# Kernel tuning notes

Hardware: AMD Instinct MI355X
Metric: run time of the kernel (lower is better)

The kernel has to match this reference:

```python
import jax, jax.numpy as jnp
import numpy as np

B = 64
D_IN = 4000            # reduced from hardcoded 40000 to fit memory budget (see notes)
N_NODES = 200
ADJ = N_NODES * N_NODES  # 40000 entries per adjacency
E_PER = ADJ // 4         # strictly > 0.75-quantile of 40000 continuous values == top 10000
NEG_SLOPE = 0.2          # GATv2Conv default leaky_relu slope
LN_EPS = 1e-5


def _gelu(x):
    return jax.nn.gelu(x, approximate=False)  # torch F.gelu default = exact erf


def _gatv2(x, src, dst, valid, Wl, bl, Wr, br, att, bias, heads, ch, concat, n):
    # PyG GATv2Conv (share_weights=False): xl = lin_l(x), xr = lin_r(x)
    xl = (x @ Wl + bl).reshape(n, heads, ch)
    xr = (x @ Wr + br).reshape(n, heads, ch)
    e = jax.nn.leaky_relu(xl[src] + xr[dst], NEG_SLOPE)        # [E,H,C]
    logits = jnp.einsum('ehc,hc->eh', e, att)                   # [E,H]
    if valid is not None:
        logits = jnp.where(valid[:, None], logits, -jnp.inf)
    m = jax.ops.segment_max(logits, dst, num_segments=n)
    m = jnp.where(jnp.isfinite(m), m, 0.0)
    ex = jnp.exp(logits - m[dst])
    if valid is not None:
        ex = jnp.where(valid[:, None], ex, 0.0)
    denom = jax.ops.segment_sum(ex, dst, num_segments=n)
    alpha = ex / (denom[dst] + 1e-16)                            # scatter-softmax per target
    out = jax.ops.segment_sum(xl[src] * alpha[..., None], dst, num_segments=n)
    out = out.reshape(n, heads * ch) if concat else out.mean(axis=1)
    return out + bias


def _forward(raw_fc, gbW, gbb, feW1, feb1, feW2, feb2, ln_g, ln_b,
             W1l, b1l, W1r, b1r, att1, bias1,
             W2l, b2l, W2r, b2r, att2, bias2,
             W3l, b3l, W3r, b3r, att3, bias3):
    b = raw_fc.shape[0]
    n = b * N_NODES
    # ---- build_graph ----
    adj = jax.nn.sigmoid(raw_fc @ gbW + gbb).reshape(b, N_NODES, N_NODES)
    adj = (adj + jnp.swapaxes(adj, 1, 2)) * 0.5
    means = adj.mean(axis=2)                    # [B,200]
    stds = jnp.std(adj, axis=2, ddof=1) + 1e-6  # torch std is unbiased
    base = jnp.stack([means, stds], axis=-1).reshape(n, 2)
    h = _gelu(base @ feW1 + feb1) @ feW2 + feb2
    mu = h.mean(-1, keepdims=True)
    var = h.var(-1, keepdims=True)
    x = (h - mu) / jnp.sqrt(var + LN_EPS) * ln_g + ln_b          # LayerNorm(16)
    _, idx = jax.lax.top_k(adj.reshape(b, ADJ), E_PER)           # [B, 10000]
    row = idx // N_NODES
    col = idx % N_NODES
    offs = (jnp.arange(b) * N_NODES)[:, None]
    src = (row + offs).reshape(-1)
    dst = (col + offs).reshape(-1)
    # ---- GAT stack (eval mode: dropout = identity) ----
    x = _gelu(_gatv2(x, src, dst, None, W1l, b1l, W1r, b1r, att1, bias1, 8, 128, True, n))
    # layers 2/3 have add_self_loops=True: remove existing self loops, append one per node
    loops = jnp.arange(n)
    src2 = jnp.concatenate([src, loops])
    dst2 = jnp.concatenate([dst, loops])
    valid2 = jnp.concatenate([src != dst, jnp.ones((n,), bool)])
    x = _gelu(_gatv2(x, src2, dst2, valid2, W2l, b2l, W2r, b2r, att2, bias2, 4, 256, True, n))
    x = _gelu(_gatv2(x, src2, dst2, valid2, W3l, b3l, W3r, b3r, att3, bias3, 1, 512, False, n))
    # global_mean_pool: exactly 200 nodes per graph, contiguous ordering
    return x.reshape(b, N_NODES, 512).mean(axis=1)


def setup_inputs() -> dict:
    key = jax.random.key(0)
    ks = jax.random.split(key, 16)
    f32 = jnp.float32
    def gl(k, shape, fan_in):
        return jax.random.normal(k, shape, f32) / np.sqrt(fan_in)
    inp = {}
    inp['raw_fc'] = jax.random.normal(ks[0], (B, D_IN), f32)
    inp['gbW'] = gl(ks[1], (D_IN, ADJ), D_IN)
    inp['gbb'] = jnp.zeros((ADJ,), f32)
    inp['feW1'] = gl(ks[2], (2, 8), 2);      inp['feb1'] = jnp.zeros((8,), f32)
    inp['feW2'] = gl(ks[3], (8, 16), 8);     inp['feb2'] = jnp.zeros((16,), f32)
    inp['ln_g'] = jnp.ones((16,), f32);      inp['ln_b'] = jnp.zeros((16,), f32)
    inp['W1l'] = gl(ks[4], (16, 8 * 128), 16);   inp['b1l'] = jnp.zeros((8 * 128,), f32)
    inp['W1r'] = gl(ks[5], (16, 8 * 128), 16);   inp['b1r'] = jnp.zeros((8 * 128,), f32)
    inp['att1'] = gl(ks[6], (8, 128), 128);      inp['bias1'] = jnp.zeros((8 * 128,), f32)
    inp['W2l'] = gl(ks[7], (1024, 4 * 256), 1024); inp['b2l'] = jnp.zeros((4 * 256,), f32)
    inp['W2r'] = gl(ks[8], (1024, 4 * 256), 1024); inp['b2r'] = jnp.zeros((4 * 256,), f32)
    inp['att2'] = gl(ks[9], (4, 256), 256);        inp['bias2'] = jnp.zeros((4 * 256,), f32)
    inp['W3l'] = gl(ks[10], (1024, 512), 1024);    inp['b3l'] = jnp.zeros((512,), f32)
    inp['W3r'] = gl(ks[11], (1024, 512), 1024);    inp['b3r'] = jnp.zeros((512,), f32)
    inp['att3'] = gl(ks[12], (1, 512), 512);       inp['bias3'] = jnp.zeros((512,), f32)
    return inp


def reference(raw_fc, gbW, gbb, feW1, feb1, feW2, feb2, ln_g, ln_b,
              W1l, b1l, W1r, b1r, att1, bias1,
              W2l, b2l, W2r, b2r, att2, bias2,
              W3l, b3l, W3r, b3r, att3, bias3):
    return _forward(raw_fc, gbW, gbb, feW1, feb1, feW2, feb2, ln_g, ln_b,
                    W1l, b1l, W1r, b1r, att1, bias1,
                    W2l, b2l, W2r, b2r, att2, bias2,
                    W3l, b3l, W3r, b3r, att3, bias3)
```

## Files before the change

### kernel.cpp

```cpp
#include <hip/hip_runtime.h>
#include <hip/hip_fp16.h>
#include <math.h>
#include <cstdint>
#include <cstddef>

#define NGRAPH 64
#define NN 200
#define ADJN 40000
#define DIN 4000
#define NNODE 12800

typedef float    f32x4 __attribute__((ext_vector_type(4)));
typedef _Float16 f16x8 __attribute__((ext_vector_type(8)));
typedef _Float16 f16x4 __attribute__((ext_vector_type(4)));
typedef _Float16 f16x2 __attribute__((ext_vector_type(2)));
typedef short    bf8v  __attribute__((ext_vector_type(8)));
typedef short    bf4v  __attribute__((ext_vector_type(4)));

union BF8U  { bf8v v; bf4v h[2]; };
union F16X8U{ f16x8 v; f16x4 h[2]; f16x2 p[4]; };

__device__ __forceinline__ unsigned short f2bf(float f) {
  unsigned u = __float_as_uint(f);
  return (unsigned short)((u + 0x7fffu + ((u >> 16) & 1u)) >> 16);
}
__device__ __forceinline__ float bf2f(unsigned short s) {
  return __uint_as_float(((unsigned)s) << 16);
}
__device__ __forceinline__ float gelu_f(float x) {
  return x * 0.5f * (1.0f + erff(x * 0.70710678118654752f));
}

#if defined(__has_builtin)
#if __has_builtin(__builtin_amdgcn_fdot2)
#define FDOT2(a, b, c) __builtin_amdgcn_fdot2((a), (b), (c), false)
#endif
#endif
#ifndef FDOT2
#define FDOT2(a, b, c) ((c) + (float)(a)[0] * (float)(b)[0] + (float)(a)[1] * (float)(b)[1])
#endif

__global__ __launch_bounds__(256) void prep_A(const float* __restrict__ A,
                                              short* __restrict__ Ahi,
                                              short* __restrict__ Alo) {
  const int i = blockIdx.x * 256 + threadIdx.x;
  const float v = A[i];
  const unsigned short h = f2bf(v);
  Ahi[i] = (short)h;
  Alo[i] = (short)f2bf(v - bf2f(h));
}

__global__ __launch_bounds__(256) void transp_all(
    const float* __restrict__ W2l, const float* __restrict__ W2r,
    const float* __restrict__ W3l, const float* __restrict__ W3r,
    _Float16* __restrict__ T2l, _Float16* __restrict__ T2r,
    _Float16* __restrict__ T3l, _Float16* __restrict__ T3r) {
  __shared__ float tile[32][33];
  const int z = blockIdx.z;
  if (z >= 2 && blockIdx.y >= 16) return;
  const float* src = (z == 0) ? W2l : (z == 1) ? W2r : (z == 2) ? W3l : W3r;
  _Float16* dst = (z == 0) ? T2l : (z == 1) ? T2r : (z == 2) ? T3l : T3r;
  const int N = (z < 2) ? 1024 : 512;
  const int K = 1024;
  const int bk = blockIdx.x * 32, bn = blockIdx.y * 32;
  const int tx = threadIdx.x & 31, ty = threadIdx.x >> 5;
#pragma unroll
  for (int r = 0; r < 32; r += 8) tile[ty + r][tx] = src[(size_t)(bk + ty + r) * N + bn + tx];
  __syncthreads();
#pragma unroll
  for (int r = 0; r < 32; r += 8)
    dst[(size_t)(bn + ty + r) * K + bk + tx] = (_Float16)tile[tx][ty + r];
}

#define BA_STEP(P, IT, W0, W1, AH, AL)                                          \
  {                                                                             \
    float wv[8] = {W0.x, W0.y, W0.z, W0.w, W1.x, W1.y, W1.z, W1.w};             \
    _Pragma("unroll") for (int q = 0; q < 8; ++q) {                             \
      unsigned short hh = f2bf(wv[q]);                                          \
      Wh[P][(wnc + q) * 44 + wk] = (short)hh;                                   \
      Wl[P][(wnc + q) * 44 + wk] = (short)f2bf(wv[q] - bf2f(hh));               \
    }                                                                           \
    const bf8v ahc = AH, alc = AL;                                              \
    if ((IT) + 2 < 125) {                                                       \
      const int k0 = ((IT) + 2) * 32;                                           \
      W0 = *(const float4*)(W + (size_t)(k0 + wk) * ADJN + n0 + wnc);           \
      W1 = *(const float4*)(W + (size_t)(k0 + wk) * ADJN + n0 + wnc + 4);       \
      AH = *(const bf8v*)(Ahi + (size_t)arow * DIN + k0 + kb);                  \
      AL = *(const bf8v*)(Alo + (size_t)arow * DIN + k0 + kb);                  \
    }                                                                           \
    __syncthreads();                                                            \
    _Pragma("unroll") for (int j = 0; j < 4; ++j) {                             \
      const int bc = (j * 16 + (lane & 15)) * 44 + kb;                          \
      BF8U bh, bl;                                                              \
      bh.h[0] = *(const bf4v*)(Wh[P] + bc);                                     \
      bh.h[1] = *(const bf4v*)(Wh[P] + bc + 4);                                 \
      bl.h[0] = *(const bf4v*)(Wl[P] + bc);                                     \
      bl.h[1] = *(const bf4v*)(Wl[P] + bc + 4);                                 \
      acc[j] = __builtin_amdgcn_mfma_f32_16x16x32_bf16(ahc, bh.v, acc[j], 0, 0, 0); \
      acc[j] = __builtin_amdgcn_mfma_f32_16x16x32_bf16(ahc, bl.v, acc[j], 0, 0, 0); \
      acc[j] = __builtin_amdgcn_mfma_f32_16x16x32_bf16(alc, bh.v, acc[j], 0, 0, 0); \
    }                                                                           \
  }

__global__ __launch_bounds__(256) void build_adj(
    const short* __restrict__ Ahi, const short* __restrict__ Alo,
    const float* __restrict__ W, const float* __restrict__ bias,
    float* __restrict__ adj) {
  __shared__ short Wh[2][64 * 44], Wl[2][64 * 44];
  const int t = threadIdx.x, wave = t >> 6, lane = t & 63;
  const int n0 = blockIdx.x * 64;
  const int wk = t >> 3, wnc = (t & 7) * 8;
  const int kb = (lane >> 4) * 8;
  const int arow = wave * 16 + (lane & 15);
  f32x4 acc[4] = {};
  float4 w0a = *(const float4*)(W + (size_t)wk * ADJN + n0 + wnc);
  float4 w1a = *(const float4*)(W + (size_t)wk * ADJN + n0 + wnc + 4);
  bf8v aha = *(const bf8v*)(Ahi + (size_t)arow * DIN + kb);
  bf8v ala = *(const bf8v*)(Alo + (size_t)arow * DIN + kb);
  float4 w0b = *(const float4*)(W + (size_t)(32 + wk) * ADJN + n0 + wnc);
  float4 w1b = *(const float4*)(W + (size_t)(32 + wk) * ADJN + n0 + wnc + 4);
  bf8v ahb = *(const bf8v*)(Ahi + (size_t)arow * DIN + 32 + kb);
  bf8v alb = *(const bf8v*)(Alo + (size_t)arow * DIN + 32 + kb);
  for (int it = 0; it < 124; it += 2) {
    BA_STEP(0, it, w0a, w1a, aha, ala)
    BA_STEP(1, it + 1, w0b, w1b, ahb, alb)
  }
  BA_STEP(0, 124, w0a, w1a, aha, ala)
#pragma unroll
  for (int j = 0; j < 4; ++j) {
    const int col = n0 + j * 16 + (lane & 15);
    const float bb = bias[col];
#pragma unroll
    for (int vv = 0; vv < 4; ++vv) {
      const int row = wave * 16 + (lane >> 4) * 4 + vv;
      float x = acc[j][vv] + bb;
      adj[(size_t)row * ADJN + col] = 1.0f / (1.0f + __expf(-x));
    }
  }
}

__global__ __launch_bounds__(256) void symmetrize(const float* __restrict__ adj,
                                                  float* __restrict__ adjS) {
  __shared__ float tl[64][65];
  const int g = blockIdx.x;
  const int i0 = (blockIdx.y >> 2) * 64, j0 = (blockIdx.y & 3) * 64;
  const int tx = threadIdx.x & 63, ty = threadIdx.x >> 6;
  const float* ag = adj + (size_t)g * ADJN;
#pragma unroll
  for (int r = 0; r < 64; r += 4) {
    const int jr = j0 + ty + r;
    tl[ty + r][tx] = (jr < NN && i0 + tx < NN) ? ag[jr * NN + i0 + tx] : 0.f;
  }
  __syncthreads();
#pragma unroll
  for (int r = 0; r < 64; r += 4) {
    const int i = i0 + ty + r, j = j0 + tx;
    if (i < NN && j < NN)
      adjS[(size_t)g * ADJN + i * NN + j] = 0.5f * (ag[i * NN + j] + tl[tx][ty + r]);
  }
}

__global__ __launch_bounds__(256) void rowstats(const float* __restrict__ adjS,
                                                float* __restrict__ meanv,
                                                float* __restrict__ stdv) {
  const int row = blockIdx.x * 4 + (threadIdx.x >> 6);
  const int lane = threadIdx.x & 63;
  const float* r = adjS + (size_t)row * NN;
  float s = 0.f, q = 0.f;
#pragma unroll
  for (int k = 0; k < 4; ++k) {
    int i = k * 64 + lane;
    if (i < NN) { float v = r[i]; s += v; q += v * v; }
  }
#pragma unroll
  for (int off = 32; off > 0; off >>= 1) { s += __shfl_xor(s, off); q += __shfl_xor(q, off); }
  if (lane == 0) {
    float m = s * (1.0f / 200.0f);
    float var = (q - 200.0f * m * m) * (1.0f / 199.0f);
    var = fmaxf(var, 0.f);
    meanv[row] = m;
    stdv[row] = sqrtf(var) + 1e-6f;
  }
}

__global__ __launch_bounds__(512) void radix_select(const float* __restrict__ adjS,
                                                    float* __restrict__ tau) {
  __shared__ unsigned hist[2048];
  __shared__ unsigned s_pref, s_cA;
  const int g = blockIdx.x, t = threadIdx.x, lane = t & 63;
  const float* v = adjS + (size_t)g * ADJN;
  unsigned prefix = 0, pmask = 0, cA = 0;
  const int shifts[3] = {20, 9, 0};
  const int widths[3] = {2048, 2048, 512};
  for (int pass = 0; pass < 3; ++pass) {
    const int nb = widths[pass], sh = shifts[pass];
    for (int i = t; i < nb; i += 512) hist[i] = 0u;
    __syncthreads();
    for (int e = t; e < ADJN; e += 512) {
      unsigned u = __float_as_uint(v[e]);
      if ((u & pmask) == prefix) atomicAdd(&hist[(u >> sh) & (nb - 1)], 1u);
    }
    __syncthreads();
    if (t < 64) {
      const int CH = nb >> 6;
      unsigned lsum = 0;
      for (int i = 0; i < CH; ++i) lsum += hist[t * CH + i];
      unsigned s = lsum;
#pragma unroll
      for (int off = 1; off < 64; off <<= 1) {
        unsigned o = __shfl_down(s, off);
        if (lane + off < 64) s += o;
      }
      const unsigned need = 10000u - cA;
      unsigned sn = __shfl_down(s, 1);
      const unsigned snext = (lane == 63) ? 0u : sn;
      if (s >= need && snext < need) {
        unsigned cum = snext;
        int b = t * CH;
        for (int i = CH - 1; i >= 0; --i) {
          unsigned hb = hist[t * CH + i];
          if (cum + hb >= need) { b = t * CH + i; break; }
          cum += hb;
        }
        s_pref = prefix | ((unsigned)b << sh);
        s_cA = cA + cum;
      }
    }
    __syncthreads();
    prefix = s_pref; cA = s_cA;
    pmask |= (unsigned)(widths[pass] - 1) << sh;
    __syncthreads();
  }
  if (t == 0) tau[g] = __uint_as_float(prefix);
}

__global__ __launch_bounds__(256) void node_mlp(
    const float* __restrict__ meanv, const float* __restrict__ stdv,
    const float* __restrict__ feW1, const float* __restrict__ feb1,
    const float* __restrict__ feW2, const float* __restrict__ feb2,
    const float* __restrict__ ln_g, const float* __restrict__ ln_b,
    float* __restrict__ x0) {
  const int n = blockIdx.x * 256 + threadIdx.x;
  const float mu = meanv[n], sd = stdv[n];
  float h1[8];
#pragma unroll
  for (int o = 0; o < 8; ++o) h1[o] = gelu_f(mu * feW1[o] + sd * feW1[8 + o] + feb1[o]);
  float h2[16]; float s = 0.f;
#pragma unroll
  for (int o = 0; o < 16; ++o) {
    float a = feb2[o];
#pragma unroll
    for (int k = 0; k < 8; ++k) a += h1[k] * feW2[k * 16 + o];
    h2[o] = a; s += a;
  }
  s *= (1.0f / 16.0f);
  float var = 0.f;
#pragma unroll
  for (int o = 0; o < 16; ++o) { float d = h2[o] - s; var += d * d; }
  var *= (1.0f / 16.0f);
  const float inv = 1.0f / sqrtf(var + 1e-5f);
#pragma unroll
  for (int o = 0; o < 16; ++o) x0[(size_t)n * 16 + o] = (h2[o] - s) * inv * ln_g[o] + ln_b[o];
}

__global__ __launch_bounds__(256) void build_lists(
    const float* __restrict__ adjS, const float* __restrict__ tau,
    int* __restrict__ cnt1, int* __restrict__ cnt2,
    unsigned char* __restrict__ list1, unsigned char* __restrict__ list2) {
  const int g = blockIdx.x >> 2, quad = blockIdx.x & 3;
  const float tv = tau[g];
  const int t = threadIdx.x, wave = t >> 6, lane = t & 63;
  for (int jj = wave; jj < 50; jj += 4) {
    const int j = quad * 50 + jj;
    const float* row = adjS + (size_t)g * ADJN + (size_t)j * NN;
    unsigned char* l1 = list1 + ((size_t)g * NN + j) * NN;
    unsigned char* l2 = list2 + ((size_t)g * NN + j) * NN;
    int c1 = 0, c2 = 0;
#pragma unroll
    for (int r = 0; r < 4; ++r) {
      int i = r * 64 + lane;
      bool p1 = false, p2 = false;
      if (i < NN) { float v = row[i]; p1 = (v >= tv); p2 = p1 && (i != j); }
      unsigned long long b1 = __ballot(p1);
      unsigned long long b2 = __ballot(p2);
      unsigned long long below = (lane == 0) ? 0ull : ((~0ull) >> (64 - lane));
      if (p1) l1[c1 + __popcll(b1 & below)] = (unsigned char)i;
      if (p2) l2[c2 + __popcll(b2 & below)] = (unsigned char)i;
      c1 += (int)__popcll(b1); c2 += (int)__popcll(b2);
    }
    if (lane == 0) {
      l2[c2] = (unsigned char)j;
      cnt1[g * NN + j] = c1;
      cnt2[g * NN + j] = c2 + 1;
    }
  }
}

__global__ __launch_bounds__(256) void lin16_mfma(
    const float* __restrict__ x0,
    const float* __restrict__ Wl, const float* __restrict__ bl,
    const float* __restrict__ Wr, const float* __restrict__ br,
    _Float16* __restrict__ outl, _Float16* __restrict__ outr) {
  __shared__ _Float16 Wt[2][1024 * 20];
  const int t = threadIdx.x, wave = t >> 6, lane = t & 63;
  const int mbase = blockIdx.x * 16;
  for (int i = t; i < 8192; i += 256) {
    const int mat = i >> 12, r = i & 4095;
    const int k = r >> 8, n4 = (r & 255) * 4;
    const float* Wsrc = mat ? Wr : Wl;
    float4 wv = *(const float4*)(Wsrc + (size_t)k * 1024 + n4);
    Wt[mat][(n4 + 0) * 20 + k] = (_Float16)wv.x;
    Wt[mat][(n4 + 1) * 20 + k] = (_Float16)wv.y;
    Wt[mat][(n4 + 2) * 20 + k] = (_Float16)wv.z;
    Wt[mat][(n4 + 3) * 20 + k] = (_Float16)wv.w;
  }
  const int mrow = lane & 15, kg = lane >> 4;
  F16X8U af;
#pragma unroll
  for (int q = 0; q < 8; ++q) af.v[q] = (_Float16)0.f;
  if (kg < 2) {
    const float* xp = x0 + (size_t)(mbase + mrow) * 16 + kg * 8;
    float4 v0 = *(const float4*)xp;
    float4 v1 = *(const float4*)(xp + 4);
    af.v[0] = (_Float16)v0.x; af.v[1] = (_Float16)v0.y;
    af.v[2] = (_Float16)v0.z; af.v[3] = (_Float16)v0.w;
    af.v[4] = (_Float16)v1.x; af.v[5] = (_Float16)v1.y;
    af.v[6] = (_Float16)v1.z; af.v[7] = (_Float16)v1.w;
  }
  __syncthreads();
#pragma unroll
  for (int mat = 0; mat < 2; ++mat) {
    const float* bias = mat ? br : bl;
    _Float16* out = mat ? outr : outl;
#pragma unroll
    for (int nt = 0; nt < 16; ++nt) {
      const int n0 = wave * 256 + nt * 16;
      F16X8U bfv;
#pragma unroll
      for (int q = 0; q < 8; ++q) bfv.v[q] = (_Float16)0.f;
      if (kg < 2) bfv.v = *(const f16x8*)(Wt[mat] + (n0 + mrow) * 20 + kg * 8);
      f32x4 acc = {};
      acc = __builtin_amdgcn_mfma_f32_16x16x32_f16(af.v, bfv.v, acc, 0, 0, 0);
      const int col = n0 + mrow;
      const float bb = bias[col];
#pragma unroll
      for (int j = 0; j < 4; ++j)
        out[(size_t)(mbase + kg * 4 + j) * 1024 + col] = (_Float16)(acc[j] + bb);
    }
  }
}

__global__ __launch_bounds__(256, 2) void gemm_nt(
    const _Float16* __restrict__ A,
    const _Float16* __restrict__ Bt0, const _Float16* __restrict__ Bt1,
    const float* __restrict__ b0, const float* __restrict__ b1,
    _Float16* __restrict__ out0, _Float16* __restrict__ out1,
    int Nhalf, int tilesPerHalf) {
  __shared__ _Float16 As[2][128 * 64];
  __shared__ _Float16 Bs[2][128 * 64];
  const int mbase = blockIdx.y * 128;
  const int hsel = blockIdx.x / tilesPerHalf;
  const int ncol0 = (blockIdx.x % tilesPerHalf) * 128;
  const _Float16* Bt = hsel ? Bt1 : Bt0;
  const float* bias = hsel ? b1 : b0;
  _Float16* out = hsel ? out1 : out0;
  const int t = threadIdx.x, wave = t >> 6, lane = t & 63;
  const int wm = wave >> 1, wn = wave & 1;
  f32x4 acc[4][4] = {};
  int crow[4], gco[4], sto[4];
#pragma unroll
  for (int q = 0; q < 4; ++q) {
    const int c = q * 256 + t;
    crow[q] = c >> 3;
    const int sl = c & 7;
    gco[q] = sl * 8;
    sto[q] = crow[q] * 64 + ((sl ^ (crow[q] & 7)) << 3);
  }
  f16x8 ra[4], rb[4];
#pragma unroll
  for (int q = 0; q < 4; ++q) {
    ra[q] = *(const f16x8*)(A + (size_t)(mbase + crow[q]) * 1024 + gco[q]);
    rb[q] = *(const f16x8*)(Bt + (size_t)(ncol0 + crow[q]) * 1024 + gco[q]);
  }
  for (int kt = 0; kt < 16; ++kt) {
    const int p = kt & 1;
#pragma unroll
    for (int q = 0; q < 4; ++q) {
      *(f16x8*)(As[p] + sto[q]) = ra[q];
      *(f16x8*)(Bs[p] + sto[q]) = rb[q];
    }
    if (kt < 15) {
      const int k0 = (kt + 1) * 64;
#pragma unroll
      for (int q = 0; q < 4; ++q) {
        ra[q] = *(const f16x8*)(A + (size_t)(mbase + crow[q]) * 1024 + k0 + gco[q]);
        rb[q] = *(const f16x8*)(Bt + (size_t)(ncol0 + crow[q]) * 1024 + k0 + gco[q]);
      }
    }
    __syncthreads();
#pragma unroll
    for (int ks = 0; ks < 2; ++ks) {
      F16X8U af[4], bfv[4];
#pragma unroll
      for (int m = 0; m < 4; ++m) {
        const int row = wm * 64 + m * 16 + (lane & 15);
        const int kk = ks * 32 + (lane >> 4) * 8;
        af[m].v = *(const f16x8*)(As[p] + row * 64 + (kk ^ ((row & 7) << 3)));
      }
#pragma unroll
      for (int j = 0; j < 4; ++j) {
        const int row = wn * 64 + j * 16 + (lane & 15);
        const int kk = ks * 32 + (lane >> 4) * 8;
        bfv[j].v = *(const f16x8*)(Bs[p] + row * 64 + (kk ^ ((row & 7) << 3)));
      }
#pragma unroll
      for (int j = 0; j < 4; ++j)
#pragma unroll
        for (int m = 0; m < 4; ++m)
          acc[m][j] = __builtin_amdgcn_mfma_f32_16x16x32_f16(af[m].v, bfv[j].v, acc[m][j], 0, 0, 0);
    }
  }
#pragma unroll
  for (int j = 0; j < 4; ++j) {
    const int col = ncol0 + wn * 64 + j * 16 + (lane & 15);
    const float bb = bias[col];
#pragma unroll
    for (int m = 0; m < 4; ++m) {
#pragma unroll
      for (int vv = 0; vv < 4; ++vv) {
        const int row = mbase + wm * 64 + m * 16 + (lane >> 4) * 4 + vv;
        out[(size_t)row * Nhalf + col] = (_Float16)(acc[m][j][vv] + bb);
      }
    }
  }
}

template <int C, int NR, int NSPLIT, int HC, bool USE_LL>
__global__ __launch_bounds__(1024, 4) void gat_layer(
    const _Float16* __restrict__ xlb, const _Float16* __restrict__ xrb,
    const float* __restrict__ attw, const float* __restrict__ biasw,
    const int* __restrict__ cnts, const unsigned char* __restrict__ lists,
    _Float16* __restrict__ outb) {
  extern __shared__ char smem[];
  constexpr int XLB = 200 * C * 2;
  constexpr int XRB = NR * C * 2;
  constexpr int AWB = 16 * 200 * 2;
  _Float16* xr_s = (_Float16*)(smem + XLB);
  _Float16* aw = (_Float16*)(smem + XLB + XRB);
  unsigned char* ll = (unsigned char*)(smem + XLB + XRB + AWB);
  unsigned* att_s = (unsigned*)(smem + XLB + XRB + AWB + (USE_LL ? 3200 : 0));
  const int g = blockIdx.x;
  const int hd = blockIdx.y / NSPLIT;
  const int range = blockIdx.y % NSPLIT;
  const int r0 = range * NR;
  const int t = threadIdx.x, wave = t >> 6, lane = t & 63;
  constexpr int GRP = (C == 128) ? 16 : 32;
  constexpr int NG = 64 / GRP;
  const int grp = lane / GRP, li = lane % GRP;

  for (int ch = t; ch < 200 * (C / 8); ch += 1024) {
    const int node = ch / (C / 8), cc = (ch % (C / 8)) * 8;
    f16x8 v = *(const f16x8*)(xlb + (size_t)(g * 200 + node) * HC + hd * C + cc);
    *(f16x8*)(smem + (((node * C + cc) * 2) ^ ((node & 15) << 4))) = v;
  }
  for (int ch = t; ch < NR * (C / 8); ch += 1024) {
    const int node = ch / (C / 8), cc = (ch % (C / 8)) * 8;
    *(f16x8*)(xr_s + node * C + cc) =
        *(const f16x8*)(xrb + (size_t)(g * 200 + r0 + node) * HC + hd * C + cc);
  }
  for (int i = t; i < C / 2; i += 1024) {
    f16x2 a;
    a[0] = (_Float16)attw[hd * C + 2 * i];
    a[1] = (_Float16)attw[hd * C + 2 * i + 1];
    att_s[i] = __builtin_bit_cast(unsigned, a);
  }
  __syncthreads();

  for (int jj = wave; jj < NR; jj += 16) {
    const int j = r0 + jj;
    const int gn = g * 200 + j;
    const int cnt = cnts[gn];
    const unsigned char* lst = lists + (size_t)gn * NN;
    float lg[4] = {-INFINITY, -INFINITY, -INFINITY, -INFINITY};
#pragma unroll
    for (int r = 0; r < 4; ++r) {
      const int e = (r << 6) + lane;
      if (e < cnt) {
        const int s = lst[e];
        if constexpr (USE_LL) ll[wave * 200 + e] = (unsigned char)s;
        const int swz = (s & 15) << 4;
        float accv[4] = {0.f, 0.f, 0.f, 0.f};
#pragma unroll
        for (int c0 = 0; c0 < C; c0 += 16) {
          const int ai = ((c0 >> 4) & 1) * 2;
          const unsigned* ap = att_s + c0 / 2;
          F16X8U xa, xb, raa, rbb;
          xa.v = *(const f16x8*)(smem + (((s * C + c0) * 2) ^ swz));
          xb.v = *(const f16x8*)(smem + (((s * C + c0 + 8) * 2) ^ swz));
          raa.v = *(const f16x8*)(xr_s + jj * C + c0);
          rbb.v = *(const f16x8*)(xr_s + jj * C + c0 + 8);
#pragma unroll
          for (int pq = 0; pq < 4; ++pq) {
            f16x2 z = xa.p[pq] + raa.p[pq];
            f16x2 zs = z * (_Float16)0.2f;
            f16x2 m = __builtin_elementwise_max(z, zs);
            accv[ai] = FDOT2(__builtin_bit_cast(f16x2, ap[pq]), m, accv[ai]);
            f16x2 z2 = xb.p[pq] + rbb.p[pq];
            f16x2 zs2 = z2 * (_Float16)0.2f;
            f16x2 m2 = __builtin_elementwise_max(z2, zs2);
            accv[ai + 1] = FDOT2(__builtin_bit_cast(f16x2, ap[4 + pq]), m2, accv[ai + 1]);
          }
        }
        lg[r] = (accv[0] + accv[1]) + (accv[2] + accv[3]);
      }
    }
    float mloc = fmaxf(fmaxf(lg[0], lg[1]), fmaxf(lg[2], lg[3]));
#pragma unroll
    for (int off = 32; off > 0; off >>= 1) mloc = fmaxf(mloc, __shfl_xor(mloc, off));
    float ex[4]; float ps = 0.f;
#pragma unroll
    for (int r = 0; r < 4; ++r) { ex[r] = __expf(lg[r] - mloc); ps += ex[r]; }
#pragma unroll
    for (int off = 32; off > 0; off >>= 1) ps += __shfl_xor(ps, off);
    const float denom = ps + 1e-16f;
#pragma unroll
    for (int r = 0; r < 4; ++r) {
      const int e = (r << 6) + lane;
      if (e < cnt) aw[wave * 200 + e] = (_Float16)(ex[r] / denom);
    }
    float o[8] = {};
    for (int e0 = 0; e0 < cnt; e0 += NG) {
      const int e = e0 + grp;
      if (e < cnt) {
        const float a = (float)aw[wave * 200 + e];
        int s;
        if constexpr (USE_LL) s = ll[wave * 200 + e]; else s = lst[e];
        const int swz = (s & 15) << 4;
        f16x8 xv = *(const f16x8*)(smem + (((s * C + li * 8) * 2) ^ swz));
#pragma unroll
        for (int q = 0; q < 8; ++q) o[q] += a * (float)xv[q];
      }
    }
#pragma unroll
    for (int q = 0; q < 8; ++q) {
      if constexpr (GRP == 16) o[q] += __shfl_xor(o[q], 16);
      o[q] += __shfl_xor(o[q], 32);
    }
    if (grp == 0) {
      const int colb = hd * C + li * 8;
      f16x8 ov;
#pragma unroll
      for (int q = 0; q < 8; ++q) ov[q] = (_Float16)gelu_f(o[q] + biasw[colb + q]);
      *(f16x8*)(outb + (size_t)gn * HC + colb) = ov;
    }
  }
}

__global__ __launch_bounds__(1024, 4) void gat_l3(
    const _Float16* __restrict__ xlb, const _Float16* __restrict__ xrb,
    const float* __restrict__ attw, const float* __restrict__ biasw,
    const int* __restrict__ cnts, const unsigned char* __restrict__ lists,
    float* __restrict__ psum) {
  extern __shared__ char smem[];
  _Float16* xr_s = (_Float16*)(smem + 51200);
  float* plog = (float*)(smem + 64000);
  unsigned* att_s = (unsigned*)(smem + 104000);
  const int g = blockIdx.x, range = blockIdx.y, r0 = range * 50;
  const int t = threadIdx.x, wave = t >> 6, lane = t & 63;
  const int grp = lane >> 4, li = lane & 15;

  for (int chunk = 0; chunk < 4; ++chunk) {
    if (chunk) __syncthreads();
    for (int ch = t; ch < 200 * 16; ch += 1024) {
      const int node = ch >> 4, cc = (ch & 15) * 8;
      *(f16x8*)(smem + (((node * 128 + cc) * 2) ^ ((node & 15) << 4))) =
          *(const f16x8*)(xlb + (size_t)(g * 200 + node) * 512 + chunk * 128 + cc);
    }
    for (int ch = t; ch < 50 * 16; ch += 1024) {
      const int node = ch >> 4, cc = (ch & 15) * 8;
      *(f16x8*)(xr_s + node * 128 + cc) =
          *(const f16x8*)(xrb + (size_t)(g * 200 + r0 + node) * 512 + chunk * 128 + cc);
    }
    for (int i = t; i < 64; i += 1024) {
      f16x2 a;
      a[0] = (_Float16)attw[chunk * 128 + 2 * i];
      a[1] = (_Float16)attw[chunk * 128 + 2 * i + 1];
      att_s[i] = __builtin_bit_cast(unsigned, a);
    }
    __syncthreads();
    for (int jj = wave; jj < 50; jj += 16) {
      const int gn = g * 200 + r0 + jj;
      const int cnt = cnts[gn];
      const unsigned char* lst = lists + (size_t)gn * NN;
#pragma unroll
      for (int r = 0; r < 4; ++r) {
        const int e = (r << 6) + lane;
        if (e < cnt) {
          const int s = lst[e];
          const int swz = (s & 15) << 4;
          float accv[4] = {0.f, 0.f, 0.f, 0.f};
#pragma unroll
          for (int c0 = 0; c0 < 128; c0 += 16) {
            const int ai = ((c0 >> 4) & 1) * 2;
            const unsigned* ap = att_s + c0 / 2;
            F16X8U xa, xb, raa, rbb;
            xa.v = *(const f16x8*)(smem + (((s * 128 + c0) * 2) ^ swz));
            xb.v = *(const f16x8*)(smem + (((s * 128 + c0 + 8) * 2) ^ swz));
            raa.v = *(const f16x8*)(xr_s + jj * 128 + c0);
            rbb.v = *(const f16x8*)(xr_s + jj * 128 + c0 + 8);
#pragma unroll
            for (int pq = 0; pq < 4; ++pq) {
              f16x2 z = xa.p[pq] + raa.p[pq];
              f16x2 zs = z * (_Float16)0.2f;
              f16x2 m = __builtin_elementwise_max(z, zs);
              accv[ai] = FDOT2(__builtin_bit_cast(f16x2, ap[pq]), m, accv[ai]);
              f16x2 z2 = xb.p[pq] + rbb.p[pq];
              f16x2 zs2 = z2 * (_Float16)0.2f;
              f16x2 m2 = __builtin_elementwise_max(z2, zs2);
              accv[ai + 1] = FDOT2(__builtin_bit_cast(f16x2, ap[4 + pq]), m2, accv[ai + 1]);
            }
          }
          const float acc = (accv[0] + accv[1]) + (accv[2] + accv[3]);
          if (chunk == 0) plog[jj * 200 + e] = acc;
          else plog[jj * 200 + e] += acc;
        }
      }
    }
  }
  __syncthreads();
  for (int jj = wave; jj < 50; jj += 16) {
    const int gn = g * 200 + r0 + jj;
    const int cnt = cnts[gn];
    float lg[4] = {-INFINITY, -INFINITY, -INFINITY, -INFINITY};
#pragma unroll
    for (int r = 0; r < 4; ++r) {
      const int e = (r << 6) + lane;
      if (e < cnt) lg[r] = plog[jj * 200 + e];
    }
    float mloc = fmaxf(fmaxf(lg[0], lg[1]), fmaxf(lg[2], lg[3]));
#pragma unroll
    for (int off = 32; off > 0; off >>= 1) mloc = fmaxf(mloc, __shfl_xor(mloc, off));
    float ex[4]; float ps = 0.f;
#pragma unroll
    for (int r = 0; r < 4; ++r) { ex[r] = __expf(lg[r] - mloc); ps += ex[r]; }
#pragma unroll
    for (int off = 32; off > 0; off >>= 1) ps += __shfl_xor(ps, off);
    const float denom = ps + 1e-16f;
#pragma unroll
    for (int r = 0; r < 4; ++r) {
      const int e = (r << 6) + lane;
      if (e < cnt) plog[jj * 200 + e] = ex[r] / denom;
    }
  }
  for (int chunk = 0; chunk < 4; ++chunk) {
    __syncthreads();
    for (int ch = t; ch < 200 * 16; ch += 1024) {
      const int node = ch >> 4, cc = (ch & 15) * 8;
      *(f16x8*)(smem + (((node * 128 + cc) * 2) ^ ((node & 15) << 4))) =
          *(const f16x8*)(xlb + (size_t)(g * 200 + node) * 512 + chunk * 128 + cc);
    }
    __syncthreads();
    float p[8] = {};
    for (int jj = wave; jj < 50; jj += 16) {
      const int gn = g * 200 + r0 + jj;
      const int cnt = cnts[gn];
      const unsigned char* lst = lists + (size_t)gn * NN;
      float o[8] = {};
      for (int e0 = 0; e0 < cnt; e0 += 4) {
        const int e = e0 + grp;
        if (e < cnt) {
          const float a = plog[jj * 200 + e];
          const int s = lst[e];
          const int swz = (s & 15) << 4;
          f16x8 xv = *(const f16x8*)(smem + (((s * 128 + li * 8) * 2) ^ swz));
#pragma unroll
          for (int q = 0; q < 8; ++q) o[q] += a * (float)xv[q];
        }
      }
#pragma unroll
      for (int q = 0; q < 8; ++q) {
        o[q] += __shfl_xor(o[q], 16);
        o[q] += __shfl_xor(o[q], 32);
      }
      if (grp == 0) {
        const int colb = chunk * 128 + li * 8;
#pragma unroll
        for (int q = 0; q < 8; ++q) p[q] += gelu_f(o[q] + biasw[colb + q]);
      }
    }
    if (grp == 0) {
      const int slot = range * 16 + wave;
      float* pd = psum + ((size_t)slot * 64 + g) * 512 + chunk * 128 + li * 8;
      float4 a0 = {p[0], p[1], p[2], p[3]};
      float4 a1 = {p[4], p[5], p[6], p[7]};
      *(float4*)pd = a0;
      *(float4*)(pd + 4) = a1;
    }
  }
}

__global__ void finalize(const float* __restrict__ psum, float* __restrict__ out) {
  const int idx = blockIdx.x * 256 + threadIdx.x;
  float s = 0.f;
#pragma unroll
  for (int k = 0; k < 64; ++k) s += psum[(size_t)k * 32768 + idx];
  out[idx] = s * 0.005f;
}

extern "C" void kernel_launch(void* const* d_in, const int* in_sizes, int n_in,
                              void* d_out, int out_size, void* d_ws, size_t ws_size,
                              hipStream_t stream) {
  const float* raw_fc = (const float*)d_in[0];
  const float* gbW = (const float*)d_in[1];
  const float* gbb = (const float*)d_in[2];
  const float* feW1 = (const float*)d_in[3];
  const float* feb1 = (const float*)d_in[4];
  const float* feW2 = (const float*)d_in[5];
  const float* feb2 = (const float*)d_in[6];
  const float* ln_g = (const float*)d_in[7];
  const float* ln_b = (const float*)d_in[8];
  const float* W1l = (const float*)d_in[9];  const float* b1l = (const float*)d_in[10];
  const float* W1r = (const float*)d_in[11]; const float* b1r = (const float*)d_in[12];
  const float* att1 = (const float*)d_in[13]; const float* bias1 = (const float*)d_in[14];
  const float* W2l = (const float*)d_in[15]; const float* b2l = (const float*)d_in[16];
  const float* W2r = (const float*)d_in[17]; const float* b2r = (const float*)d_in[18];
  const float* att2 = (const float*)d_in[19]; const float* bias2 = (const float*)d_in[20];
  const float* W3l = (const float*)d_in[21]; const float* b3l = (const float*)d_in[22];
  const float* W3r = (const float*)d_in[23]; const float* b3r = (const float*)d_in[24];
  const float* att3 = (const float*)d_in[25]; const float* bias3 = (const float*)d_in[26];

  if (ws_size < 121000000) return;

  char* w = (char*)d_ws;
  float* adj   = (float*)(w + 0);
  float* adjS  = (float*)(w + 10240000);
  float* meanv = (float*)(w + 20480000);
  float* stdv  = (float*)(w + 20531200);
  float* tau   = (float*)(w + 20582400);
  float* x0    = (float*)(w + 20582656);
  int* cnt1    = (int*)(w + 21401856);
  int* cnt2    = (int*)(w + 21453056);
  unsigned char* list1 = (unsigned char*)(w + 21504256);
  unsigned char* list2 = (unsigned char*)(w + 24064256);
  _Float16* bufA = (_Float16*)(w + 26624256);
  _Float16* bufB = (_Float16*)(w + 52838656);
  _Float16* bufC = (_Float16*)(w + 79053056);
  float* psum = (float*)(w + 105267456);
  short* Ahi  = (short*)(w + 113656064);
  short* Alo  = (short*)(w + 114168064);
  _Float16* Wt2l = (_Float16*)(w + 114680064);
  _Float16* Wt2r = (_Float16*)(w + 116777216);
  _Float16* Wt3l = (_Float16*)(w + 118874368);
  _Float16* Wt3r = (_Float16*)(w + 119922944);

  const int SMEM_L1 = 112256;
  const int SMEM_L2 = 160512;
  const int SMEM_L3 = 104256;
  hipFuncSetAttribute((const void*)gat_layer<128, 200, 1, 1024, true>,
                      hipFuncAttributeMaxDynamicSharedMemorySize, SMEM_L1);
  hipFuncSetAttribute((const void*)gat_layer<256, 100, 2, 1024, false>,
                      hipFuncAttributeMaxDynamicSharedMemorySize, SMEM_L2);
  hipFuncSetAttribute((const void*)gat_l3,
                      hipFuncAttributeMaxDynamicSharedMemorySize, SMEM_L3);

  prep_A<<<1000, 256, 0, stream>>>(raw_fc, Ahi, Alo);
  transp_all<<<dim3(32, 32, 4), 256, 0, stream>>>(W2l, W2r, W3l, W3r, Wt2l, Wt2r, Wt3l, Wt3r);
  build_adj<<<625, 256, 0, stream>>>(Ahi, Alo, gbW, gbb, adj);
  symmetrize<<<dim3(64, 16), 256, 0, stream>>>(adj, adjS);
  rowstats<<<3200, 256, 0, stream>>>(adjS, meanv, stdv);
  radix_select<<<64, 512, 0, stream>>>(adjS, tau);
  node_mlp<<<50, 256, 0, stream>>>(meanv, stdv, feW1, feb1, feW2, feb2, ln_g, ln_b, x0);
  build_lists<<<256, 256, 0, stream>>>(adjS, tau, cnt1, cnt2, list1, list2);
  lin16_mfma<<<800, 256, 0, stream>>>(x0, W1l, b1l, W1r, b1r, bufA, bufB);
  gat_layer<128, 200, 1, 1024, true><<<dim3(64, 8), 1024, SMEM_L1, stream>>>(
      bufA, bufB, att1, bias1, cnt1, list1, bufC);
  gemm_nt<<<dim3(16, 100), 256, 0, stream>>>(bufC, Wt2l, Wt2r, b2l, b2r, bufA, bufB, 1024, 8);
  gat_layer<256, 100, 2, 1024, false><<<dim3(64, 8), 1024, SMEM_L2, stream>>>(
      bufA, bufB, att2, bias2, cnt2, list2, bufC);
  gemm_nt<<<dim3(8, 100), 256, 0, stream>>>(bufC, Wt3l, Wt3r, b3l, b3r, bufA, bufB, 512, 4);
  gat_l3<<<dim3(64, 4), 1024, SMEM_L3, stream>>>(bufA, bufB, att3, bias3, cnt2, list2, psum);
  finalize<<<128, 256, 0, stream>>>(psum, (float*)d_out);
}
```

Baseline: 1.009 ms.

## Fuse radix select with list building, fuse node MLP into lin16, restructure pipelines

Merges radix_select and build_lists into one kernel that builds edge lists right after finding the threshold, and uses four privatized histogram copies with 1024 threads. Folds node_mlp into the layer-1 linear kernel, and halves that kernel's shared weight buffer by loading Wl and Wr in turn. Reorders build_adj so the bf16 split conversion of the next tile overlaps the current MFMAs, and moves gemm_nt's prefetch to after the barrier. gat_layer now streams xr rows through a per-wave register buffer instead of staging them in shared memory, dropping the NSPLIT split, so layer 2 runs one block per head with less shared memory. These remove launches and intermediate buffers, but the fused list kernel has only 64 blocks.

```diff
diff --git a/kernel.cpp b/kernel.cpp
--- a/kernel.cpp
+++ b/kernel.cpp
@@ -72,35 +72,34 @@
     dst[(size_t)(bn + ty + r) * K + bk + tx] = (_Float16)tile[tx][ty + r];
 }
 
-#define BA_STEP(P, IT, W0, W1, AH, AL)                                          \
-  {                                                                             \
-    float wv[8] = {W0.x, W0.y, W0.z, W0.w, W1.x, W1.y, W1.z, W1.w};             \
+#define BA_CONV(PB, W0, W1)                                                     \
+  { float wv[8] = {W0.x, W0.y, W0.z, W0.w, W1.x, W1.y, W1.z, W1.w};             \
     _Pragma("unroll") for (int q = 0; q < 8; ++q) {                             \
       unsigned short hh = f2bf(wv[q]);                                          \
-      Wh[P][(wnc + q) * 44 + wk] = (short)hh;                                   \
-      Wl[P][(wnc + q) * 44 + wk] = (short)f2bf(wv[q] - bf2f(hh));               \
-    }                                                                           \
-    const bf8v ahc = AH, alc = AL;                                              \
-    if ((IT) + 2 < 125) {                                                       \
-      const int k0 = ((IT) + 2) * 32;                                           \
-      W0 = *(const float4*)(W + (size_t)(k0 + wk) * ADJN + n0 + wnc);           \
-      W1 = *(const float4*)(W + (size_t)(k0 + wk) * ADJN + n0 + wnc + 4);       \
-      AH = *(const bf8v*)(Ahi + (size_t)arow * DIN + k0 + kb);                  \
-      AL = *(const bf8v*)(Alo + (size_t)arow * DIN + k0 + kb);                  \
-    }                                                                           \
-    __syncthreads();                                                            \
-    _Pragma("unroll") for (int j = 0; j < 4; ++j) {                             \
-      const int bc = (j * 16 + (lane & 15)) * 44 + kb;                          \
-      BF8U bh, bl;                                                              \
-      bh.h[0] = *(const bf4v*)(Wh[P] + bc);                                     \
-      bh.h[1] = *(const bf4v*)(Wh[P] + bc + 4);                                 \
-      bl.h[0] = *(const bf4v*)(Wl[P] + bc);                                     \
-      bl.h[1] = *(const bf4v*)(Wl[P] + bc + 4);                                 \
-      acc[j] = __builtin_amdgcn_mfma_f32_16x16x32_bf16(ahc, bh.v, acc[j], 0, 0, 0); \
-      acc[j] = __builtin_amdgcn_mfma_f32_16x16x32_bf16(ahc, bl.v, acc[j], 0, 0, 0); \
-      acc[j] = __builtin_amdgcn_mfma_f32_16x16x32_bf16(alc, bh.v, acc[j], 0, 0, 0); \
-    }                                                                           \
-  }
+      Wh[PB][(wnc + q) * 44 + wk] = (short)hh;                                  \
+      Wl[PB][(wnc + q) * 44 + wk] = (short)f2bf(wv[q] - bf2f(hh));              \
+    } }
+
+#define BA_MFMA(PB, AHC, ALC)                                                   \
+  _Pragma("unroll") for (int j = 0; j < 4; ++j) {                               \
+    const int bc = (j * 16 + (lane & 15)) * 44 + kb;                            \
+    BF8U bh, bl;                                                                \
+    bh.h[0] = *(const bf4v*)(Wh[PB] + bc);                                      \
+    bh.h[1] = *(const bf4v*)(Wh[PB] + bc + 4);                                  \
+    bl.h[0] = *(const bf4v*)(Wl[PB] + bc);                                      \
+    bl.h[1] = *(const bf4v*)(Wl[PB] + bc + 4);                                  \
+    acc[j] = __builtin_amdgcn_mfma_f32_16x16x32_bf16(AHC, bh.v, acc[j], 0, 0, 0); \
+    acc[j] = __builtin_amdgcn_mfma_f32_16x16x32_bf16(AHC, bl.v, acc[j], 0, 0, 0); \
+    acc[j] = __builtin_amdgcn_mfma_f32_16x16x32_bf16(ALC, bh.v, acc[j], 0, 0, 0); \
+  }
+
+#define BA_LOADW(W0, W1, K0)                                                    \
+  W0 = *(const float4*)(W + (size_t)((K0) + wk) * ADJN + n0 + wnc);             \
+  W1 = *(const float4*)(W + (size_t)((K0) + wk) * ADJN + n0 + wnc + 4);
+
+#define BA_LOADA(AH, AL, K0)                                                    \
+  AH = *(const bf8v*)(Ahi + (size_t)arow * DIN + (K0) + kb);                    \
+  AL = *(const bf8v*)(Alo + (size_t)arow * DIN + (K0) + kb);
 
 __global__ __launch_bounds__(256) void build_adj(
     const short* __restrict__ Ahi, const short* __restrict__ Alo,
@@ -113,19 +112,39 @@
   const int kb = (lane >> 4) * 8;
   const int arow = wave * 16 + (lane & 15);
   f32x4 acc[4] = {};
-  float4 w0a = *(const float4*)(W + (size_t)wk * ADJN + n0 + wnc);
-  float4 w1a = *(const float4*)(W + (size_t)wk * ADJN + n0 + wnc + 4);
-  bf8v aha = *(const bf8v*)(Ahi + (size_t)arow * DIN + kb);
-  bf8v ala = *(const bf8v*)(Alo + (size_t)arow * DIN + kb);
-  float4 w0b = *(const float4*)(W + (size_t)(32 + wk) * ADJN + n0 + wnc);
-  float4 w1b = *(const float4*)(W + (size_t)(32 + wk) * ADJN + n0 + wnc + 4);
-  bf8v ahb = *(const bf8v*)(Ahi + (size_t)arow * DIN + 32 + kb);
-  bf8v alb = *(const bf8v*)(Alo + (size_t)arow * DIN + 32 + kb);
+  float4 w0s0, w1s0, w0s1, w1s1;
+  bf8v ahs0, als0, ahs1, als1;
+  BA_LOADW(w0s0, w1s0, 0)
+  BA_LOADA(ahs0, als0, 0)
+  BA_LOADW(w0s1, w1s1, 32)
+  BA_LOADA(ahs1, als1, 32)
+  BA_CONV(0, w0s0, w1s0)
   for (int it = 0; it < 124; it += 2) {
-    BA_STEP(0, it, w0a, w1a, aha, ala)
-    BA_STEP(1, it + 1, w0b, w1b, ahb, alb)
-  }
-  BA_STEP(0, 124, w0a, w1a, aha, ala)
+    __syncthreads();
+    {
+      const bf8v ahc = ahs0, alc = als0;
+      if (it + 2 < 125) {
+        const int k2 = (it + 2) * 32;
+        BA_LOADW(w0s0, w1s0, k2)
+        BA_LOADA(ahs0, als0, k2)
+      }
+      BA_MFMA(0, ahc, alc)
+      BA_CONV(1, w0s1, w1s1)
+    }
+    __syncthreads();
+    {
+      const bf8v ahc = ahs1, alc = als1;
+      if (it + 3 < 125) {
+        const int k2 = (it + 3) * 32;
+        BA_LOADW(w0s1, w1s1, k2)
+        BA_LOADA(ahs1, als1, k2)
+      }
+      BA_MFMA(1, ahc, alc)
+      if (it + 2 < 125) BA_CONV(0, w0s0, w1s0)
+    }
+  }
+  __syncthreads();
+  BA_MFMA(0, ahs0, als0)
 #pragma unroll
   for (int j = 0; j < 4; ++j) {
     const int col = n0 + j * 16 + (lane & 15);
@@ -183,28 +202,34 @@
   }
 }
 
-__global__ __launch_bounds__(512) void radix_select(const float* __restrict__ adjS,
-                                                    float* __restrict__ tau) {
-  __shared__ unsigned hist[2048];
+__global__ __launch_bounds__(1024) void radix_lists(
+    const float* __restrict__ adjS,
+    int* __restrict__ cnt1, int* __restrict__ cnt2,
+    unsigned char* __restrict__ list1, unsigned char* __restrict__ list2) {
+  __shared__ unsigned hist[4 * 2048];
   __shared__ unsigned s_pref, s_cA;
-  const int g = blockIdx.x, t = threadIdx.x, lane = t & 63;
+  const int g = blockIdx.x, t = threadIdx.x, lane = t & 63, wave = t >> 6;
   const float* v = adjS + (size_t)g * ADJN;
   unsigned prefix = 0, pmask = 0, cA = 0;
   const int shifts[3] = {20, 9, 0};
   const int widths[3] = {2048, 2048, 512};
   for (int pass = 0; pass < 3; ++pass) {
     const int nb = widths[pass], sh = shifts[pass];
-    for (int i = t; i < nb; i += 512) hist[i] = 0u;
-    __syncthreads();
-    for (int e = t; e < ADJN; e += 512) {
+    for (int i = t; i < 8192; i += 1024) hist[i] = 0u;
+    __syncthreads();
+    const int cpy = (lane & 3) * 2048;
+    for (int e = t; e < ADJN; e += 1024) {
       unsigned u = __float_as_uint(v[e]);
-      if ((u & pmask) == prefix) atomicAdd(&hist[(u >> sh) & (nb - 1)], 1u);
+      if ((u & pmask) == prefix) atomicAdd(&hist[cpy + ((u >> sh) & (nb - 1))], 1u);
     }
     __syncthreads();
     if (t < 64) {
       const int CH = nb >> 6;
       unsigned lsum = 0;
-      for (int i = 0; i < CH; ++i) lsum += hist[t * CH + i];
+      for (int i = 0; i < CH; ++i) {
+        const int b = t * CH + i;
+        lsum += hist[b] + hist[2048 + b] + hist[4096 + b] + hist[6144 + b];
+      }
       unsigned s = lsum;
 #pragma unroll
       for (int off = 1; off < 64; off <<= 1) {
@@ -216,13 +241,14 @@
       const unsigned snext = (lane == 63) ? 0u : sn;
       if (s >= need && snext < need) {
         unsigned cum = snext;
-        int b = t * CH;
+        int bsel = t * CH;
         for (int i = CH - 1; i >= 0; --i) {
-          unsigned hb = hist[t * CH + i];
-          if (cum + hb >= need) { b = t * CH + i; break; }
+          const int b = t * CH + i;
+          unsigned hb = hist[b] + hist[2048 + b] + hist[4096 + b] + hist[6144 + b];
+          if (cum + hb >= need) { bsel = b; break; }
           cum += hb;
         }
-        s_pref = prefix | ((unsigned)b << sh);
+        s_pref = prefix | ((unsigned)bsel << sh);
         s_cA = cA + cum;
       }
     }
@@ -231,47 +257,8 @@
     pmask |= (unsigned)(widths[pass] - 1) << sh;
     __syncthreads();
   }
-  if (t == 0) tau[g] = __uint_as_float(prefix);
-}
-
-__global__ __launch_bounds__(256) void node_mlp(
-    const float* __restrict__ meanv, const float* __restrict__ stdv,
-    const float* __restrict__ feW1, const float* __restrict__ feb1,
-    const float* __restrict__ feW2, const float* __restrict__ feb2,
-    const float* __restrict__ ln_g, const float* __restrict__ ln_b,
-    float* __restrict__ x0) {
-  const int n = blockIdx.x * 256 + threadIdx.x;
-  const float mu = meanv[n], sd = stdv[n];
-  float h1[8];
-#pragma unroll
-  for (int o = 0; o < 8; ++o) h1[o] = gelu_f(mu * feW1[o] + sd * feW1[8 + o] + feb1[o]);
-  float h2[16]; float s = 0.f;
-#pragma unroll
-  for (int o = 0; o < 16; ++o) {
-    float a = feb2[o];
-#pragma unroll
-    for (int k = 0; k < 8; ++k) a += h1[k] * feW2[k * 16 + o];
-    h2[o] = a; s += a;
-  }
-  s *= (1.0f / 16.0f);
-  float var = 0.f;
-#pragma unroll
-  for (int o = 0; o < 16; ++o) { float d = h2[o] - s; var += d * d; }
-  var *= (1.0f / 16.0f);
-  const float inv = 1.0f / sqrtf(var + 1e-5f);
-#pragma unroll
-  for (int o = 0; o < 16; ++o) x0[(size_t)n * 16 + o] = (h2[o] - s) * inv * ln_g[o] + ln_b[o];
-}
-
-__global__ __launch_bounds__(256) void build_lists(
-    const float* __restrict__ adjS, const float* __restrict__ tau,
-    int* __restrict__ cnt1, int* __restrict__ cnt2,
-    unsigned char* __restrict__ list1, unsigned char* __restrict__ list2) {
-  const int g = blockIdx.x >> 2, quad = blockIdx.x & 3;
-  const float tv = tau[g];
-  const int t = threadIdx.x, wave = t >> 6, lane = t & 63;
-  for (int jj = wave; jj < 50; jj += 4) {
-    const int j = quad * 50 + jj;
+  const float tv = __uint_as_float(prefix);
+  for (int j = wave; j < NN; j += 16) {
     const float* row = adjS + (size_t)g * ADJN + (size_t)j * NN;
     unsigned char* l1 = list1 + ((size_t)g * NN + j) * NN;
     unsigned char* l2 = list2 + ((size_t)g * NN + j) * NN;
@@ -280,7 +267,7 @@
     for (int r = 0; r < 4; ++r) {
       int i = r * 64 + lane;
       bool p1 = false, p2 = false;
-      if (i < NN) { float v = row[i]; p1 = (v >= tv); p2 = p1 && (i != j); }
+      if (i < NN) { float vv = row[i]; p1 = (vv >= tv); p2 = p1 && (i != j); }
       unsigned long long b1 = __ballot(p1);
       unsigned long long b2 = __ballot(p2);
       unsigned long long below = (lane == 0) ? 0ull : ((~0ull) >> (64 - lane));
@@ -296,40 +283,60 @@
   }
 }
 
-__global__ __launch_bounds__(256) void lin16_mfma(
-    const float* __restrict__ x0,
+__global__ __launch_bounds__(256) void lin16_fused(
+    const float* __restrict__ meanv, const float* __restrict__ stdv,
+    const float* __restrict__ feW1, const float* __restrict__ feb1,
+    const float* __restrict__ feW2, const float* __restrict__ feb2,
+    const float* __restrict__ ln_g, const float* __restrict__ ln_b,
     const float* __restrict__ Wl, const float* __restrict__ bl,
     const float* __restrict__ Wr, const float* __restrict__ br,
     _Float16* __restrict__ outl, _Float16* __restrict__ outr) {
-  __shared__ _Float16 Wt[2][1024 * 20];
+  __shared__ _Float16 Wt[1024 * 20];
+  __shared__ float x0s[16][17];
   const int t = threadIdx.x, wave = t >> 6, lane = t & 63;
   const int mbase = blockIdx.x * 16;
-  for (int i = t; i < 8192; i += 256) {
-    const int mat = i >> 12, r = i & 4095;
-    const int k = r >> 8, n4 = (r & 255) * 4;
-    const float* Wsrc = mat ? Wr : Wl;
-    float4 wv = *(const float4*)(Wsrc + (size_t)k * 1024 + n4);
-    Wt[mat][(n4 + 0) * 20 + k] = (_Float16)wv.x;
-    Wt[mat][(n4 + 1) * 20 + k] = (_Float16)wv.y;
-    Wt[mat][(n4 + 2) * 20 + k] = (_Float16)wv.z;
-    Wt[mat][(n4 + 3) * 20 + k] = (_Float16)wv.w;
-  }
+  {
+    const int n = t >> 4, o = t & 15;
+    const float mu = meanv[mbase + n], sd = stdv[mbase + n];
+    float h1[8];
+#pragma unroll
+    for (int k = 0; k < 8; ++k) h1[k] = gelu_f(mu * feW1[k] + sd * feW1[8 + k] + feb1[k]);
+    float h2 = feb2[o];
+#pragma unroll
+    for (int k = 0; k < 8; ++k) h2 += h1[k] * feW2[k * 16 + o];
+    float s = h2;
+#pragma unroll
+    for (int off = 1; off < 16; off <<= 1) s += __shfl_xor(s, off);
+    s *= (1.0f / 16.0f);
+    const float d = h2 - s;
+    float vv = d * d;
+#pragma unroll
+    for (int off = 1; off < 16; off <<= 1) vv += __shfl_xor(vv, off);
+    vv *= (1.0f / 16.0f);
+    x0s[n][o] = d * (1.0f / sqrtf(vv + 1e-5f)) * ln_g[o] + ln_b[o];
+  }
+  __syncthreads();
   const int mrow = lane & 15, kg = lane >> 4;
   F16X8U af;
 #pragma unroll
   for (int q = 0; q < 8; ++q) af.v[q] = (_Float16)0.f;
   if (kg < 2) {
-    const float* xp = x0 + (size_t)(mbase + mrow) * 16 + kg * 8;
-    float4 v0 = *(const float4*)xp;
-    float4 v1 = *(const float4*)(xp + 4);
-    af.v[0] = (_Float16)v0.x; af.v[1] = (_Float16)v0.y;
-    af.v[2] = (_Float16)v0.z; af.v[3] = (_Float16)v0.w;
-    af.v[4] = (_Float16)v1.x; af.v[5] = (_Float16)v1.y;
-    af.v[6] = (_Float16)v1.z; af.v[7] = (_Float16)v1.w;
-  }
-  __syncthreads();
+#pragma unroll
+    for (int q = 0; q < 8; ++q) af.v[q] = (_Float16)x0s[mrow][kg * 8 + q];
+  }
 #pragma unroll
   for (int mat = 0; mat < 2; ++mat) {
+    if (mat) __syncthreads();
+    const float* Wsrc = mat ? Wr : Wl;
+    for (int i = t; i < 4096; i += 256) {
+      const int k = i >> 8, n4 = (i & 255) * 4;
+      float4 wv = *(const float4*)(Wsrc + (size_t)k * 1024 + n4);
+      Wt[(n4 + 0) * 20 + k] = (_Float16)wv.x;
+      Wt[(n4 + 1) * 20 + k] = (_Float16)wv.y;
+      Wt[(n4 + 2) * 20 + k] = (_Float16)wv.z;
+      Wt[(n4 + 3) * 20 + k] = (_Float16)wv.w;
+    }
+    __syncthreads();
     const float* bias = mat ? br : bl;
     _Float16* out = mat ? outr : outl;
 #pragma unroll
@@ -338,7 +345,7 @@
       F16X8U bfv;
 #pragma unroll
       for (int q = 0; q < 8; ++q) bfv.v[q] = (_Float16)0.f;
-      if (kg < 2) bfv.v = *(const f16x8*)(Wt[mat] + (n0 + mrow) * 20 + kg * 8);
+      if (kg < 2) bfv.v = *(const f16x8*)(Wt + (n0 + mrow) * 20 + kg * 8);
       f32x4 acc = {};
       acc = __builtin_amdgcn_mfma_f32_16x16x32_f16(af.v, bfv.v, acc, 0, 0, 0);
       const int col = n0 + mrow;
@@ -389,6 +396,7 @@
       *(f16x8*)(As[p] + sto[q]) = ra[q];
       *(f16x8*)(Bs[p] + sto[q]) = rb[q];
     }
+    __syncthreads();
     if (kt < 15) {
       const int k0 = (kt + 1) * 64;
 #pragma unroll
@@ -397,7 +405,6 @@
         rb[q] = *(const f16x8*)(Bt + (size_t)(ncol0 + crow[q]) * 1024 + k0 + gco[q]);
       }
     }
-    __syncthreads();
 #pragma unroll
     for (int ks = 0; ks < 2; ++ks) {
       F16X8U af[4], bfv[4];
@@ -435,7 +442,7 @@
   }
 }
 
-template <int C, int NR, int NSPLIT, int HC, bool USE_LL>
+template <int C, int HC, bool USE_LL>
 __global__ __launch_bounds__(1024, 4) void gat_layer(
     const _Float16* __restrict__ xlb, const _Float16* __restrict__ xrb,
     const float* __restrict__ attw, const float* __restrict__ biasw,
@@ -443,16 +450,13 @@
     _Float16* __restrict__ outb) {
   extern __shared__ char smem[];
   constexpr int XLB = 200 * C * 2;
-  constexpr int XRB = NR * C * 2;
-  constexpr int AWB = 16 * 200 * 2;
+  constexpr int XRW = 16 * C * 2;
   _Float16* xr_s = (_Float16*)(smem + XLB);
-  _Float16* aw = (_Float16*)(smem + XLB + XRB);
-  unsigned char* ll = (unsigned char*)(smem + XLB + XRB + AWB);
-  unsigned* att_s = (unsigned*)(smem + XLB + XRB + AWB + (USE_LL ? 3200 : 0));
+  _Float16* aw = (_Float16*)(smem + XLB + XRW);
+  unsigned char* ll = (unsigned char*)(smem + XLB + XRW + 6400);
+  unsigned* att_s = (unsigned*)(smem + XLB + XRW + 6400 + (USE_LL ? 3200 : 0));
   const int g = blockIdx.x;
-  const int hd = blockIdx.y / NSPLIT;
-  const int range = blockIdx.y % NSPLIT;
-  const int r0 = range * NR;
+  const int hd = blockIdx.y;
   const int t = threadIdx.x, wave = t >> 6, lane = t & 63;
   constexpr int GRP = (C == 128) ? 16 : 32;
   constexpr int NG = 64 / GRP;
@@ -462,11 +466,6 @@
     const int node = ch / (C / 8), cc = (ch % (C / 8)) * 8;
     f16x8 v = *(const f16x8*)(xlb + (size_t)(g * 200 + node) * HC + hd * C + cc);
     *(f16x8*)(smem + (((node * C + cc) * 2) ^ ((node & 15) << 4))) = v;
-  }
-  for (int ch = t; ch < NR * (C / 8); ch += 1024) {
-    const int node = ch / (C / 8), cc = (ch % (C / 8)) * 8;
-    *(f16x8*)(xr_s + node * C + cc) =
-        *(const f16x8*)(xrb + (size_t)(g * 200 + r0 + node) * HC + hd * C + cc);
   }
   for (int i = t; i < C / 2; i += 1024) {
     f16x2 a;
@@ -476,11 +475,20 @@
   }
   __syncthreads();
 
-  for (int jj = wave; jj < NR; jj += 16) {
-    const int j = r0 + jj;
-    const int gn = g * 200 + j;
+  _Float16* xr_w = xr_s + wave * C;
+  f16x8 xrreg;
+  if (lane < C / 8)
+    xrreg = *(const f16x8*)(xrb + (size_t)(g * 200 + wave) * HC + hd * C + lane * 8);
+
+  for (int jj = wave; jj < 200; jj += 16) {
+    const int gn = g * 200 + jj;
     const int cnt = cnts[gn];
     const unsigned char* lst = lists + (size_t)gn * NN;
+    if (lane < C / 8) {
+      *(f16x8*)(xr_w + lane * 8) = xrreg;
+      if (jj + 16 < 200)
+        xrreg = *(const f16x8*)(xrb + (size_t)(gn + 16) * HC + hd * C + lane * 8);
+    }
     float lg[4] = {-INFINITY, -INFINITY, -INFINITY, -INFINITY};
 #pragma unroll
     for (int r = 0; r < 4; ++r) {
@@ -497,8 +505,8 @@
           F16X8U xa, xb, raa, rbb;
           xa.v = *(const f16x8*)(smem + (((s * C + c0) * 2) ^ swz));
           xb.v = *(const f16x8*)(smem + (((s * C + c0 + 8) * 2) ^ swz));
-          raa.v = *(const f16x8*)(xr_s + jj * C + c0);
-          rbb.v = *(const f16x8*)(xr_s + jj * C + c0 + 8);
+          raa.v = *(const f16x8*)(xr_w + c0);
+          rbb.v = *(const f16x8*)(xr_w + c0 + 8);
 #pragma unroll
           for (int pq = 0; pq < 4; ++pq) {
             f16x2 z = xa.p[pq] + raa.p[pq];
@@ -736,8 +744,6 @@
   float* adjS  = (float*)(w + 10240000);
   float* meanv = (float*)(w + 20480000);
   float* stdv  = (float*)(w + 20531200);
-  float* tau   = (float*)(w + 20582400);
-  float* x0    = (float*)(w + 20582656);
   int* cnt1    = (int*)(w + 21401856);
   int* cnt2    = (int*)(w + 21453056);
   unsigned char* list1 = (unsigned char*)(w + 21504256);
@@ -753,12 +759,12 @@
   _Float16* Wt3l = (_Float16*)(w + 118874368);
   _Float16* Wt3r = (_Float16*)(w + 119922944);
 
-  const int SMEM_L1 = 112256;
-  const int SMEM_L2 = 160512;
+  const int SMEM_L1 = 65152;
+  const int SMEM_L2 = 117504;
   const int SMEM_L3 = 104256;
-  hipFuncSetAttribute((const void*)gat_layer<128, 200, 1, 1024, true>,
+  hipFuncSetAttribute((const void*)gat_layer<128, 1024, true>,
                       hipFuncAttributeMaxDynamicSharedMemorySize, SMEM_L1);
-  hipFuncSetAttribute((const void*)gat_layer<256, 100, 2, 1024, false>,
+  hipFuncSetAttribute((const void*)gat_layer<256, 1024, false>,
                       hipFuncAttributeMaxDynamicSharedMemorySize, SMEM_L2);
   hipFuncSetAttribute((const void*)gat_l3,
                       hipFuncAttributeMaxDynamicSharedMemorySize, SMEM_L3);
@@ -768,14 +774,13 @@
   build_adj<<<625, 256, 0, stream>>>(Ahi, Alo, gbW, gbb, adj);
   symmetrize<<<dim3(64, 16), 256, 0, stream>>>(adj, adjS);
   rowstats<<<3200, 256, 0, stream>>>(adjS, meanv, stdv);
-  radix_select<<<64, 512, 0, stream>>>(adjS, tau);
-  node_mlp<<<50, 256, 0, stream>>>(meanv, stdv, feW1, feb1, feW2, feb2, ln_g, ln_b, x0);
-  build_lists<<<256, 256, 0, stream>>>(adjS, tau, cnt1, cnt2, list1, list2);
-  lin16_mfma<<<800, 256, 0, stream>>>(x0, W1l, b1l, W1r, b1r, bufA, bufB);
-  gat_layer<128, 200, 1, 1024, true><<<dim3(64, 8), 1024, SMEM_L1, stream>>>(
+  radix_lists<<<64, 1024, 0, stream>>>(adjS, cnt1, cnt2, list1, list2);
+  lin16_fused<<<800, 256, 0, stream>>>(meanv, stdv, feW1, feb1, feW2, feb2, ln_g, ln_b,
+                                       W1l, b1l, W1r, b1r, bufA, bufB);
+  gat_layer<128, 1024, true><<<dim3(64, 8), 1024, SMEM_L1, stream>>>(
       bufA, bufB, att1, bias1, cnt1, list1, bufC);
   gemm_nt<<<dim3(16, 100), 256, 0, stream>>>(bufC, Wt2l, Wt2r, b2l, b2r, bufA, bufB, 1024, 8);
-  gat_layer<256, 100, 2, 1024, false><<<dim3(64, 8), 1024, SMEM_L2, stream>>>(
+  gat_layer<256, 1024, false><<<dim3(64, 4), 1024, SMEM_L2, stream>>>(
       bufA, bufB, att2, bias2, cnt2, list2, bufC);
   gemm_nt<<<dim3(8, 100), 256, 0, stream>>>(bufC, Wt3l, Wt3r, b3l, b3r, bufA, bufB, 512, 4);
   gat_l3<<<dim3(64, 4), 1024, SMEM_L3, stream>>>(bufA, bufB, att3, bias3, cnt2, list2, psum);
```

Measured after the change: 976.7 us. 1.03x faster.
